# Kernel optimization log

Measured on AMD Instinct MI355X. Metric: run time of the kernel, lower is better.

## Reference

```python
import jax, jax.numpy as jnp
import numpy as np


def setup_inputs() -> dict:
    key = jax.random.key(0)
    x = jax.random.normal(key, (8, 48, 48, 48, 64), dtype=jnp.float32)
    gamma = jnp.float32(1e-4)  # matches tf.Variable(0.0001)
    return {"x": x, "gamma": gamma}


def reference(x, gamma):
    # x: (B, W, D, H, C)
    B, W, D, H, C = x.shape
    N = W * D * H
    # Keras Reshape((C, -1)) is a row-major flatten of (W, D, H, C) -> (C, N).
    # NOTE: this is NOT a channels-first transpose; it is a raw reshape,
    # exactly as the original module computes it.
    K = x.reshape(B, C, N)                      # (B, C, N)
    # Q = K^T and J = K^T in the original, so m1 = K@Q and m2 = K@J are both
    # the same Gram matrix G = K @ K^T. Compute it once.
    G = jnp.einsum('bcn,bdn->bcd', K, K)        # (B, C, C)
    m3 = jnp.einsum('bcd,bde->bce', G, G)       # (B, C, C)
    affinity = jax.nn.sigmoid(m3)               # (B, C, C)
    weights = jnp.einsum('bcd,bdn->bcn', affinity, K)  # (B, C, N)
    weights = weights.reshape(B, W, D, H, C)
    return gamma * weights + x
```

## Files before the change

kernel.cpp:

```cpp
#include <hip/hip_runtime.h>

#define NCOL 110592
#define NCH  64
#define CN   (NCOL * NCH)
#define NB   8

typedef __attribute__((ext_vector_type(8))) __bf16 bf16x8;
typedef __attribute__((ext_vector_type(4))) float  f32x4;

__global__ __launch_bounds__(256) void k_gram(const float* __restrict__ x,
                                              float* __restrict__ part,
                                              int steps) {
    const int b     = blockIdx.y;
    const int chunk = blockIdx.x;
    const int tid   = threadIdx.x;
    const int w     = tid >> 6;
    const int lane  = tid & 63;
    const int r     = lane & 15;
    const int q     = lane >> 4;

    const float* xb = x + (size_t)b * CN;

    f32x4 acc0 = {0.f, 0.f, 0.f, 0.f};
    f32x4 acc1 = {0.f, 0.f, 0.f, 0.f};
    f32x4 acc2 = {0.f, 0.f, 0.f, 0.f};
    f32x4 acc3 = {0.f, 0.f, 0.f, 0.f};

    const int kbase = chunk * steps * 32 + q * 8;

    for (int s = 0; s < steps; ++s) {
        const int k0 = kbase + s * 32;
        bf16x8 frag[4];
#pragma unroll
        for (int i = 0; i < 4; ++i) {
            const float* p = xb + (size_t)(i * 16 + r) * NCOL + k0;
            f32x4 lo = *(const f32x4*)p;
            f32x4 hi = *(const f32x4*)(p + 4);
            bf16x8 f;
            f[0] = (__bf16)lo[0]; f[1] = (__bf16)lo[1];
            f[2] = (__bf16)lo[2]; f[3] = (__bf16)lo[3];
            f[4] = (__bf16)hi[0]; f[5] = (__bf16)hi[1];
            f[6] = (__bf16)hi[2]; f[7] = (__bf16)hi[3];
            frag[i] = f;
        }
        bf16x8 af = (w == 0) ? frag[0] : (w == 1) ? frag[1]
                  : (w == 2) ? frag[2] : frag[3];
        acc0 = __builtin_amdgcn_mfma_f32_16x16x32_bf16(af, frag[0], acc0, 0, 0, 0);
        acc1 = __builtin_amdgcn_mfma_f32_16x16x32_bf16(af, frag[1], acc1, 0, 0, 0);
        acc2 = __builtin_amdgcn_mfma_f32_16x16x32_bf16(af, frag[2], acc2, 0, 0, 0);
        acc3 = __builtin_amdgcn_mfma_f32_16x16x32_bf16(af, frag[3], acc3, 0, 0, 0);
    }

    float* pp = part + (size_t)(b * gridDim.x + chunk) * 4096;
#pragma unroll
    for (int rr = 0; rr < 4; ++rr) {
        const int m = w * 16 + q * 4 + rr;
        pp[m * 64 + (0 * 16 + r)] = acc0[rr];
        pp[m * 64 + (1 * 16 + r)] = acc1[rr];
        pp[m * 64 + (2 * 16 + r)] = acc2[rr];
        pp[m * 64 + (3 * 16 + r)] = acc3[rr];
    }
}

__global__ __launch_bounds__(256) void k_reduce(const float* __restrict__ part,
                                                float* __restrict__ G,
                                                int chunks) {
    const int b    = blockIdx.y;
    const int cq   = threadIdx.x & 63;
    const int ph   = threadIdx.x >> 6;
    const int cell = blockIdx.x * 256 + cq * 4;

    f32x4 s = {0.f, 0.f, 0.f, 0.f};
    for (int p = ph; p < chunks; p += 4) {
        const f32x4 v = *(const f32x4*)(part + (size_t)(b * chunks + p) * 4096 + cell);
        s[0] += v[0]; s[1] += v[1]; s[2] += v[2]; s[3] += v[3];
    }

    __shared__ f32x4 red[4][64];
    red[ph][cq] = s;
    __syncthreads();
    if (ph == 0) {
        const f32x4 a = red[0][cq], b1 = red[1][cq];
        const f32x4 c = red[2][cq], d = red[3][cq];
        f32x4 o;
        o[0] = a[0] + b1[0] + c[0] + d[0];
        o[1] = a[1] + b1[1] + c[1] + d[1];
        o[2] = a[2] + b1[2] + c[2] + d[2];
        o[3] = a[3] + b1[3] + c[3] + d[3];
        *(f32x4*)(G + b * 4096 + cell) = o;
    }
}

__global__ __launch_bounds__(256) void k_affinity(const float* __restrict__ G,
                                                  const float* __restrict__ gptr,
                                                  float* __restrict__ A) {
    const int b = blockIdx.x;
    __shared__ float Gs[64 * 65];
    const float* Gb = G + b * 4096;
    for (int i = threadIdx.x; i < 1024; i += 256) {
        const f32x4 v = *(const f32x4*)(Gb + i * 4);
        const int row = i >> 4;
        const int col = (i & 15) * 4;
        Gs[row * 65 + col + 0] = v[0];
        Gs[row * 65 + col + 1] = v[1];
        Gs[row * 65 + col + 2] = v[2];
        Gs[row * 65 + col + 3] = v[3];
    }
    __syncthreads();
    const float gamma = gptr[0];
    for (int id = threadIdx.x; id < 4096; id += 256) {
        const int c = id >> 6, e = id & 63;
        float dot = 0.f;
#pragma unroll
        for (int d = 0; d < 64; ++d)
            dot += Gs[c * 65 + d] * Gs[e * 65 + d];
        const float aff = 1.0f / (1.0f + __expf(-dot));
        A[b * 4096 + id] = gamma * aff + ((c == e) ? 1.0f : 0.0f);
    }
}

__global__ __launch_bounds__(256, 4) void k_apply(const float* __restrict__ x,
                                                  const float* __restrict__ A,
                                                  float* __restrict__ out) {
    const int b = blockIdx.y;
    const int n = blockIdx.x * 256 + threadIdx.x;
    const float* xb = x + (size_t)b * CN + n;
    float*       ob = out + (size_t)b * CN + n;
    const float* Ab = A + b * 4096;

    float acc[64];
#pragma unroll
    for (int c = 0; c < 64; ++c) acc[c] = 0.f;

#pragma unroll 8
    for (int d = 0; d < 64; ++d) {
        const float k = xb[(size_t)d * NCOL];
#pragma unroll
        for (int c = 0; c < 64; ++c)
            acc[c] += Ab[d * 64 + c] * k;
    }

#pragma unroll
    for (int c = 0; c < 64; ++c)
        ob[(size_t)c * NCOL] = acc[c];
}

extern "C" void kernel_launch(void* const* d_in, const int* in_sizes, int n_in,
                              void* d_out, int out_size, void* d_ws, size_t ws_size,
                              hipStream_t stream) {
    const float* x    = (const float*)d_in[0];
    const float* gptr = (const float*)d_in[1];
    float*       out  = (float*)d_out;
    float*       ws   = (float*)d_ws;

    int chunks = 128;
    auto need = [](int ch) { return (size_t)(8 * ch + 16) * 4096 * 4; };
    if (ws_size < need(128)) chunks = 64;
    if (ws_size < need(64))  chunks = 32;
    if (ws_size < need(32))  chunks = 8;
    if (ws_size < need(8))   chunks = 2;
    const int steps = 3456 / chunks;

    float* part = ws;
    float* G    = ws + (size_t)8 * chunks * 4096;
    float* Aff  = G + 8 * 4096;

    k_gram    <<<dim3(chunks, 8), 256, 0, stream>>>(x, part, steps);
    k_reduce  <<<dim3(16, 8),     256, 0, stream>>>(part, G, chunks);
    k_affinity<<<8,               256, 0, stream>>>(G, gptr, Aff);
    k_apply   <<<dim3(432, 8),    256, 0, stream>>>(x, Aff, out);
}
```

Before: 510.7 us.

## Prefetch next step in gram kernel, vectorize apply kernel, raise chunk count

The gram kernel now software-pipelines its global loads, fetching the next step's fp32 tiles into registers while the current step's bf16 MFMAs run, and gains an occupancy hint. The apply kernel is restructured so each thread handles four consecutive columns with float4 loads and stores, and each wavefront covers 16 output channels instead of one thread holding all 64. The default gram chunk count rises to 216 to spread work over more blocks, at the cost of more partial sums to reduce and more workspace. Extra prefetch registers could pressure occupancy.

Result: slower. 608.1 us (+19.1%).

```diff
diff --git a/kernel.cpp b/kernel.cpp
--- a/kernel.cpp
+++ b/kernel.cpp
@@ -8,9 +8,9 @@
 typedef __attribute__((ext_vector_type(8))) __bf16 bf16x8;
 typedef __attribute__((ext_vector_type(4))) float  f32x4;
 
-__global__ __launch_bounds__(256) void k_gram(const float* __restrict__ x,
-                                              float* __restrict__ part,
-                                              int steps) {
+__global__ __launch_bounds__(256, 4) void k_gram(const float* __restrict__ x,
+                                                 float* __restrict__ part,
+                                                 int steps) {
     const int b     = blockIdx.y;
     const int chunk = blockIdx.x;
     const int tid   = threadIdx.x;
@@ -28,19 +28,34 @@
 
     const int kbase = chunk * steps * 32 + q * 8;
 
+    f32x4 lo[4], hi[4];
+#pragma unroll
+    for (int i = 0; i < 4; ++i) {
+        const float* p = xb + (size_t)(i * 16 + r) * NCOL + kbase;
+        lo[i] = *(const f32x4*)p;
+        hi[i] = *(const f32x4*)(p + 4);
+    }
+
     for (int s = 0; s < steps; ++s) {
-        const int k0 = kbase + s * 32;
+        f32x4 nlo[4], nhi[4];
+        if (s + 1 < steps) {
+            const int k1 = kbase + (s + 1) * 32;
+#pragma unroll
+            for (int i = 0; i < 4; ++i) {
+                const float* p = xb + (size_t)(i * 16 + r) * NCOL + k1;
+                nlo[i] = *(const f32x4*)p;
+                nhi[i] = *(const f32x4*)(p + 4);
+            }
+        }
+
         bf16x8 frag[4];
 #pragma unroll
         for (int i = 0; i < 4; ++i) {
-            const float* p = xb + (size_t)(i * 16 + r) * NCOL + k0;
-            f32x4 lo = *(const f32x4*)p;
-            f32x4 hi = *(const f32x4*)(p + 4);
             bf16x8 f;
-            f[0] = (__bf16)lo[0]; f[1] = (__bf16)lo[1];
-            f[2] = (__bf16)lo[2]; f[3] = (__bf16)lo[3];
-            f[4] = (__bf16)hi[0]; f[5] = (__bf16)hi[1];
-            f[6] = (__bf16)hi[2]; f[7] = (__bf16)hi[3];
+            f[0] = (__bf16)lo[i][0]; f[1] = (__bf16)lo[i][1];
+            f[2] = (__bf16)lo[i][2]; f[3] = (__bf16)lo[i][3];
+            f[4] = (__bf16)hi[i][0]; f[5] = (__bf16)hi[i][1];
+            f[6] = (__bf16)hi[i][2]; f[7] = (__bf16)hi[i][3];
             frag[i] = f;
         }
         bf16x8 af = (w == 0) ? frag[0] : (w == 1) ? frag[1]
@@ -49,6 +64,9 @@
         acc1 = __builtin_amdgcn_mfma_f32_16x16x32_bf16(af, frag[1], acc1, 0, 0, 0);
         acc2 = __builtin_amdgcn_mfma_f32_16x16x32_bf16(af, frag[2], acc2, 0, 0, 0);
         acc3 = __builtin_amdgcn_mfma_f32_16x16x32_bf16(af, frag[3], acc3, 0, 0, 0);
+
+#pragma unroll
+        for (int i = 0; i < 4; ++i) { lo[i] = nlo[i]; hi[i] = nhi[i]; }
     }
 
     float* pp = part + (size_t)(b * gridDim.x + chunk) * 4096;
@@ -122,27 +140,35 @@
 __global__ __launch_bounds__(256, 4) void k_apply(const float* __restrict__ x,
                                                   const float* __restrict__ A,
                                                   float* __restrict__ out) {
-    const int b = blockIdx.y;
-    const int n = blockIdx.x * 256 + threadIdx.x;
+    const int b    = blockIdx.y;
+    const int w    = threadIdx.x >> 6;
+    const int lane = threadIdx.x & 63;
+    const int n    = blockIdx.x * 256 + lane * 4;
+
     const float* xb = x + (size_t)b * CN + n;
-    float*       ob = out + (size_t)b * CN + n;
-    const float* Ab = A + b * 4096;
+    float*       ob = out + (size_t)b * CN + (size_t)(w * 16) * NCOL + n;
+    const float* Ab = A + b * 4096 + w * 16;
 
-    float acc[64];
+    f32x4 acc[16];
 #pragma unroll
-    for (int c = 0; c < 64; ++c) acc[c] = 0.f;
+    for (int c = 0; c < 16; ++c) acc[c] = (f32x4){0.f, 0.f, 0.f, 0.f};
 
-#pragma unroll 8
+#pragma unroll 4
     for (int d = 0; d < 64; ++d) {
-        const float k = xb[(size_t)d * NCOL];
+        const f32x4 k = *(const f32x4*)(xb + (size_t)d * NCOL);
 #pragma unroll
-        for (int c = 0; c < 64; ++c)
-            acc[c] += Ab[d * 64 + c] * k;
+        for (int c = 0; c < 16; ++c) {
+            const float a = Ab[d * 64 + c];
+            acc[c][0] += a * k[0];
+            acc[c][1] += a * k[1];
+            acc[c][2] += a * k[2];
+            acc[c][3] += a * k[3];
+        }
     }
 
 #pragma unroll
-    for (int c = 0; c < 64; ++c)
-        ob[(size_t)c * NCOL] = acc[c];
+    for (int c = 0; c < 16; ++c)
+        *(f32x4*)(ob + (size_t)c * NCOL) = acc[c];
 }
 
 extern "C" void kernel_launch(void* const* d_in, const int* in_sizes, int n_in,
@@ -153,8 +179,9 @@
     float*       out  = (float*)d_out;
     float*       ws   = (float*)d_ws;
 
-    int chunks = 128;
+    int chunks = 216;
     auto need = [](int ch) { return (size_t)(8 * ch + 16) * 4096 * 4; };
+    if (ws_size < need(216)) chunks = 128;
     if (ws_size < need(128)) chunks = 64;
     if (ws_size < need(64))  chunks = 32;
     if (ws_size < need(32))  chunks = 8;
```
